# Optimization experiments

Hardware: AMD Instinct MI355X
Metric: run time of the kernel (lower is better)

Reference implementation:

```python
import jax, jax.numpy as jnp
import numpy as np


def setup_inputs() -> dict:
    key = jax.random.key(0)
    k1, k2 = jax.random.split(key)
    B, T, V = 256, 128, 512
    x = jax.random.normal(k1, (B, T, V), dtype=jnp.float32)
    targets = jax.random.randint(k2, (B, T), 0, V)
    return {"x": x, "targets": targets, "sup_batchsize": 256}


def reference(x, targets, sup_batchsize):
    # Faithful vectorization of InfoNCELoss.loss_fun (the per-i Python loop).
    x = jnp.clip(x, -30.0, 30.0)
    B, T, V = x.shape
    S = int(sup_batchsize)
    tgt = targets[:S]  # [S, T] target sequences used as positives/negatives

    # terms[i, b] = sum_t x[b, t, tgt[i, t]]  (gather each target sequence across the whole batch)
    gathered = jnp.take_along_axis(x[None], tgt[:, None, :, None], axis=3)  # [S, B, T, 1]
    terms = gathered[..., 0].sum(axis=-1)  # [S, B]

    denom = jax.nn.logsumexp(terms, axis=1)  # [S]
    numerators = terms[jnp.arange(S), jnp.arange(S)]  # terms[i, i] = own-sequence score
    losses = numerators - denom  # [S], per-row InfoNCE log-prob

    # coef[i, b] = 1{b == i} - softmax_b(terms[i, :])
    indicator = (jnp.arange(B)[None, :] == jnp.arange(S)[:, None]).astype(x.dtype)
    coef = indicator - jax.nn.softmax(terms, axis=1)  # [S, B]

    # grad[b, t, v] = sum_i 1{v == tgt[i, t]} * coef[i, b]  (scatter-add, no [S,T,V] one-hot)
    t_idx = jnp.arange(T)[None, :]  # broadcasts with tgt to [S, T]
    grad = jnp.zeros_like(x).at[:, t_idx, tgt].add(
        jnp.broadcast_to(coef.T[:, :, None], (B, S, T))
    )

    total_loss = losses.sum()  # InfoNCEFunction.forward returns sum(loss)
    return total_loss, grad
```

## Files before the change

kernel.cpp:

```cpp
#include <hip/hip_runtime.h>


#define TT 128
#define VV 512
#define QSPLIT 8
#define TQ (TT / QSPLIT)
#define TC 8

typedef float f4 __attribute__((ext_vector_type(4)));

__global__ __launch_bounds__(256) void terms_kernel(
    const float* __restrict__ x, const int* __restrict__ tgt,
    float* __restrict__ partial) {
  int bid = blockIdx.x;
  int b = bid & 255, q = bid >> 8, s = threadIdx.x;
  __shared__ __align__(16) float xch[TC * VV];
  const float* xb = x + ((size_t)b * TT + q * TQ) * VV;
  int4 tg[4];
#pragma unroll
  for (int k = 0; k < 4; ++k)
    tg[k] = ((const int4*)(tgt + (size_t)s * TT + q * TQ))[k];
  float acc = 0.f;
#pragma unroll
  for (int c = 0; c < 2; ++c) {
    const float4* src = (const float4*)(xb + c * TC * VV);
    float4* dst = (float4*)xch;
#pragma unroll
    for (int k = 0; k < 4; ++k) {
      float4 v = src[s + k * 256];
      v.x = fminf(fmaxf(v.x, -30.f), 30.f);
      v.y = fminf(fmaxf(v.y, -30.f), 30.f);
      v.z = fminf(fmaxf(v.z, -30.f), 30.f);
      v.w = fminf(fmaxf(v.w, -30.f), 30.f);
      dst[s + k * 256] = v;
    }
    __syncthreads();
    int4 a0 = tg[2 * c], a1 = tg[2 * c + 1];
    acc += xch[0 * VV + a0.x] + xch[1 * VV + a0.y] +
           xch[2 * VV + a0.z] + xch[3 * VV + a0.w] +
           xch[4 * VV + a1.x] + xch[5 * VV + a1.y] +
           xch[6 * VV + a1.z] + xch[7 * VV + a1.w];
    __syncthreads();
  }
  partial[(size_t)((q << 8) + b) * 256 + s] = acc;
}

__global__ __launch_bounds__(256) void softmax_kernel(
    const float* __restrict__ partial, float* __restrict__ coefT,
    float* __restrict__ losses) {
  int s = blockIdx.x, b = threadIdx.x;
  int w = b >> 6, lane = b & 63;
  float t = 0.f;
#pragma unroll
  for (int q = 0; q < QSPLIT; ++q)
    t += partial[(size_t)((q << 8) + b) * 256 + s];
  float m = t;
#pragma unroll
  for (int off = 32; off; off >>= 1) m = fmaxf(m, __shfl_xor(m, off));
  __shared__ float wm[4], ws[4];
  if (lane == 0) wm[w] = m;
  __syncthreads();
  m = fmaxf(fmaxf(wm[0], wm[1]), fmaxf(wm[2], wm[3]));
  float e = expf(t - m);
  float ss = e;
#pragma unroll
  for (int off = 32; off; off >>= 1) ss += __shfl_xor(ss, off);
  if (lane == 0) ws[w] = ss;
  __syncthreads();
  float sum = ws[0] + ws[1] + ws[2] + ws[3];
  coefT[(b << 8) + s] = (b == s ? 1.f : 0.f) - e / sum;
  if (b == s) losses[s] = (t - m) - logf(sum);
}

__global__ __launch_bounds__(256) void grad_kernel(
    const float* __restrict__ coefT, const int* __restrict__ tgt,
    const float* __restrict__ losses, float* __restrict__ out) {
  int j = blockIdx.x, s = threadIdx.x;
  int w = s >> 6, lane = s & 63;
  int b = j >> 4, t0 = (j & 15) << 3;
  __shared__ __align__(16) float rows[TC * VV + 1];
  __shared__ double dred[4];
  f4* rz = (f4*)rows;
  f4 zero = {0.f, 0.f, 0.f, 0.f};
#pragma unroll
  for (int k = 0; k < 4; ++k) rz[s + k * 256] = zero;
  if (s == 0) rows[TC * VV] = 0.f;

  float c = coefT[(b << 8) + s];
  int4 tg0 = *(const int4*)(tgt + (size_t)s * TT + t0);
  int4 tg1 = *(const int4*)(tgt + (size_t)s * TT + t0 + 4);

  float bc = 0.f;
  if (j > 0) {
    int R = j * 8 - 1;
    int bh = R >> 7, th = R & 127;
    if (tgt[(size_t)s * TT + th] == VV - 1) bc = coefT[(bh << 8) + s];
  }
  double ls = 0.0;
  if (j == 0) ls = (double)losses[s];

  __syncthreads();
  atomicAdd(&rows[1 + 0 * VV + tg0.x], c);
  atomicAdd(&rows[1 + 1 * VV + tg0.y], c);
  atomicAdd(&rows[1 + 2 * VV + tg0.z], c);
  atomicAdd(&rows[1 + 3 * VV + tg0.w], c);
  atomicAdd(&rows[1 + 4 * VV + tg1.x], c);
  atomicAdd(&rows[1 + 5 * VV + tg1.y], c);
  atomicAdd(&rows[1 + 6 * VV + tg1.z], c);
  atomicAdd(&rows[1 + 7 * VV + tg1.w], c);
#pragma unroll
  for (int off = 32; off; off >>= 1) bc += __shfl_xor(bc, off);
  if (j > 0 && lane == 0) atomicAdd(&rows[0], bc);
  if (j == 0) {
#pragma unroll
    for (int off = 32; off; off >>= 1) ls += __shfl_xor(ls, off);
    if (lane == 0) dred[w] = ls;
  }
  __syncthreads();
  if (j == 0 && s == 0) rows[0] = (float)(dred[0] + dred[1] + dred[2] + dred[3]);
  __syncthreads();

  f4* go = (f4*)(out + (size_t)j * 4096);
#pragma unroll
  for (int k = 0; k < 4; ++k)
    __builtin_nontemporal_store(rz[s + k * 256], &go[s + k * 256]);
  if (j == 4095 && s == 0) out[(size_t)4096 * 4096] = rows[TC * VV];
}

extern "C" void kernel_launch(void* const* d_in, const int* in_sizes, int n_in,
                              void* d_out, int out_size, void* d_ws, size_t ws_size,
                              hipStream_t stream) {
  const float* x = (const float*)d_in[0];
  const int* tgt = (const int*)d_in[1];
  float* out = (float*)d_out;

  float* partial = (float*)d_ws;
  float* coefT = partial + QSPLIT * 256 * 256;
  float* losses = coefT + 256 * 256;

  terms_kernel<<<dim3(2048), dim3(256), 0, stream>>>(x, tgt, partial);
  softmax_kernel<<<dim3(256), dim3(256), 0, stream>>>(partial, coefT, losses);
  grad_kernel<<<dim3(4096), dim3(256), 0, stream>>>(coefT, tgt, losses, out);
}
```

Baseline: 165.4 us.

## Fuse three kernels into one cooperative launch with grid syncs and LDS direct loads

```diff
diff --git a/kernel.cpp b/kernel.cpp
--- a/kernel.cpp
+++ b/kernel.cpp
@@ -1,4 +1,7 @@
 #include <hip/hip_runtime.h>
+#include <hip/hip_cooperative_groups.h>
+
+namespace cg = cooperative_groups;
 
 
 #define TT 128
@@ -8,6 +11,131 @@
 #define TC 8
 
 typedef float f4 __attribute__((ext_vector_type(4)));
+
+__device__ __forceinline__ float clip30(float v) {
+  return fminf(fmaxf(v, -30.f), 30.f);
+}
+
+__device__ __forceinline__ void gload16(const float* g, float* l) {
+  __builtin_amdgcn_global_load_lds(
+      (const __attribute__((address_space(1))) unsigned int*)g,
+      (__attribute__((address_space(3))) unsigned int*)l, 16, 0, 0);
+}
+
+__global__ __launch_bounds__(256) void fused_kernel(
+    const float* __restrict__ x, const int* __restrict__ tgt,
+    float* __restrict__ partial, float* __restrict__ coefT,
+    float* __restrict__ losses, float* __restrict__ out) {
+  cg::grid_group gg = cg::this_grid();
+  int bid = blockIdx.x, s = threadIdx.x;
+  int w = s >> 6, lane = s & 63;
+  __shared__ __align__(16) float smem[TC * VV + 1];
+  __shared__ double dred[4];
+  __shared__ float wred[8];
+
+  {
+    int b = bid & 255, q = bid >> 8;
+    const float* xb = x + ((size_t)b * TT + q * TQ) * VV;
+    int4 tg[4];
+#pragma unroll
+    for (int k = 0; k < 4; ++k)
+      tg[k] = ((const int4*)(tgt + (size_t)s * TT + q * TQ))[k];
+    float acc = 0.f;
+#pragma unroll
+    for (int c = 0; c < 2; ++c) {
+      const float* src = xb + c * TC * VV;
+#pragma unroll
+      for (int k = 0; k < 4; ++k)
+        gload16(src + 4 * (s + k * 256), &smem[4 * (s + k * 256)]);
+      __syncthreads();
+      int4 a0 = tg[2 * c], a1 = tg[2 * c + 1];
+      acc += clip30(smem[0 * VV + a0.x]) + clip30(smem[1 * VV + a0.y]) +
+             clip30(smem[2 * VV + a0.z]) + clip30(smem[3 * VV + a0.w]) +
+             clip30(smem[4 * VV + a1.x]) + clip30(smem[5 * VV + a1.y]) +
+             clip30(smem[6 * VV + a1.z]) + clip30(smem[7 * VV + a1.w]);
+      __syncthreads();
+    }
+    partial[(size_t)((q << 8) + b) * 256 + s] = acc;
+  }
+
+  gg.sync();
+
+  if (bid < 256) {
+    int row = bid, b = s;
+    float t = 0.f;
+#pragma unroll
+    for (int q = 0; q < QSPLIT; ++q)
+      t += partial[(size_t)((q << 8) + b) * 256 + row];
+    float m = t;
+#pragma unroll
+    for (int off = 32; off; off >>= 1) m = fmaxf(m, __shfl_xor(m, off));
+    if (lane == 0) wred[w] = m;
+    __syncthreads();
+    m = fmaxf(fmaxf(wred[0], wred[1]), fmaxf(wred[2], wred[3]));
+    float e = expf(t - m);
+    float ssum = e;
+#pragma unroll
+    for (int off = 32; off; off >>= 1) ssum += __shfl_xor(ssum, off);
+    if (lane == 0) wred[4 + w] = ssum;
+    __syncthreads();
+    float sum = wred[4] + wred[5] + wred[6] + wred[7];
+    coefT[(b << 8) + row] = (b == row ? 1.f : 0.f) - e / sum;
+    if (b == row) losses[row] = (t - m) - logf(sum);
+  }
+
+  gg.sync();
+
+#pragma unroll 1
+  for (int tt = 0; tt < 2; ++tt) {
+    int j = (bid << 1) | tt;
+    int b = j >> 4, t0 = (j & 15) << 3;
+    f4* rz = (f4*)smem;
+    f4 zero = {0.f, 0.f, 0.f, 0.f};
+#pragma unroll
+    for (int k = 0; k < 4; ++k) rz[s + k * 256] = zero;
+    if (s == 0) smem[TC * VV] = 0.f;
+
+    float c = coefT[(b << 8) + s];
+    int4 tg0 = *(const int4*)(tgt + (size_t)s * TT + t0);
+    int4 tg1 = *(const int4*)(tgt + (size_t)s * TT + t0 + 4);
+
+    float bc = 0.f;
+    if (j > 0) {
+      int R = j * 8 - 1;
+      int bh = R >> 7, th = R & 127;
+      if (tgt[(size_t)s * TT + th] == VV - 1) bc = coefT[(bh << 8) + s];
+    }
+    double ls = 0.0;
+    if (j == 0) ls = (double)losses[s];
+
+    __syncthreads();
+    atomicAdd(&smem[1 + 0 * VV + tg0.x], c);
+    atomicAdd(&smem[1 + 1 * VV + tg0.y], c);
+    atomicAdd(&smem[1 + 2 * VV + tg0.z], c);
+    atomicAdd(&smem[1 + 3 * VV + tg0.w], c);
+    atomicAdd(&smem[1 + 4 * VV + tg1.x], c);
+    atomicAdd(&smem[1 + 5 * VV + tg1.y], c);
+    atomicAdd(&smem[1 + 6 * VV + tg1.z], c);
+    atomicAdd(&smem[1 + 7 * VV + tg1.w], c);
+#pragma unroll
+    for (int off = 32; off; off >>= 1) bc += __shfl_xor(bc, off);
+    if (j > 0 && lane == 0) atomicAdd(&smem[0], bc);
+    if (j == 0) {
+#pragma unroll
+      for (int off = 32; off; off >>= 1) ls += __shfl_xor(ls, off);
+      if (lane == 0) dred[w] = ls;
+    }
+    __syncthreads();
+    if (j == 0 && s == 0) smem[0] = (float)(dred[0] + dred[1] + dred[2] + dred[3]);
+    __syncthreads();
+
+    f4* go = (f4*)(out + (size_t)j * 4096);
+#pragma unroll
+    for (int k = 0; k < 4; ++k)
+      __builtin_nontemporal_store(rz[s + k * 256], &go[s + k * 256]);
+    if (j == 4095 && s == 0) out[(size_t)4096 * 4096] = smem[TC * VV];
+  }
+}
 
 __global__ __launch_bounds__(256) void terms_kernel(
     const float* __restrict__ x, const int* __restrict__ tgt,
@@ -23,23 +151,16 @@
   float acc = 0.f;
 #pragma unroll
   for (int c = 0; c < 2; ++c) {
-    const float4* src = (const float4*)(xb + c * TC * VV);
-    float4* dst = (float4*)xch;
-#pragma unroll
-    for (int k = 0; k < 4; ++k) {
-      float4 v = src[s + k * 256];
-      v.x = fminf(fmaxf(v.x, -30.f), 30.f);
-      v.y = fminf(fmaxf(v.y, -30.f), 30.f);
-      v.z = fminf(fmaxf(v.z, -30.f), 30.f);
-      v.w = fminf(fmaxf(v.w, -30.f), 30.f);
-      dst[s + k * 256] = v;
-    }
+    const float* src = xb + c * TC * VV;
+#pragma unroll
+    for (int k = 0; k < 4; ++k)
+      gload16(src + 4 * (s + k * 256), &xch[4 * (s + k * 256)]);
     __syncthreads();
     int4 a0 = tg[2 * c], a1 = tg[2 * c + 1];
-    acc += xch[0 * VV + a0.x] + xch[1 * VV + a0.y] +
-           xch[2 * VV + a0.z] + xch[3 * VV + a0.w] +
-           xch[4 * VV + a1.x] + xch[5 * VV + a1.y] +
-           xch[6 * VV + a1.z] + xch[7 * VV + a1.w];
+    acc += clip30(xch[0 * VV + a0.x]) + clip30(xch[1 * VV + a0.y]) +
+           clip30(xch[2 * VV + a0.z]) + clip30(xch[3 * VV + a0.w]) +
+           clip30(xch[4 * VV + a1.x]) + clip30(xch[5 * VV + a1.y]) +
+           clip30(xch[6 * VV + a1.z]) + clip30(xch[7 * VV + a1.w]);
     __syncthreads();
   }
   partial[(size_t)((q << 8) + b) * 256 + s] = acc;
@@ -48,12 +169,12 @@
 __global__ __launch_bounds__(256) void softmax_kernel(
     const float* __restrict__ partial, float* __restrict__ coefT,
     float* __restrict__ losses) {
-  int s = blockIdx.x, b = threadIdx.x;
+  int row = blockIdx.x, b = threadIdx.x;
   int w = b >> 6, lane = b & 63;
   float t = 0.f;
 #pragma unroll
   for (int q = 0; q < QSPLIT; ++q)
-    t += partial[(size_t)((q << 8) + b) * 256 + s];
+    t += partial[(size_t)((q << 8) + b) * 256 + row];
   float m = t;
 #pragma unroll
   for (int off = 32; off; off >>= 1) m = fmaxf(m, __shfl_xor(m, off));
@@ -62,14 +183,14 @@
   __syncthreads();
   m = fmaxf(fmaxf(wm[0], wm[1]), fmaxf(wm[2], wm[3]));
   float e = expf(t - m);
-  float ss = e;
-#pragma unroll
-  for (int off = 32; off; off >>= 1) ss += __shfl_xor(ss, off);
-  if (lane == 0) ws[w] = ss;
+  float ssum = e;
+#pragma unroll
+  for (int off = 32; off; off >>= 1) ssum += __shfl_xor(ssum, off);
+  if (lane == 0) ws[w] = ssum;
   __syncthreads();
   float sum = ws[0] + ws[1] + ws[2] + ws[3];
-  coefT[(b << 8) + s] = (b == s ? 1.f : 0.f) - e / sum;
-  if (b == s) losses[s] = (t - m) - logf(sum);
+  coefT[(b << 8) + row] = (b == row ? 1.f : 0.f) - e / sum;
+  if (b == row) losses[row] = (t - m) - logf(sum);
 }
 
 __global__ __launch_bounds__(256) void grad_kernel(
@@ -138,7 +259,13 @@
   float* coefT = partial + QSPLIT * 256 * 256;
   float* losses = coefT + 256 * 256;
 
-  terms_kernel<<<dim3(2048), dim3(256), 0, stream>>>(x, tgt, partial);
-  softmax_kernel<<<dim3(256), dim3(256), 0, stream>>>(partial, coefT, losses);
-  grad_kernel<<<dim3(4096), dim3(256), 0, stream>>>(coefT, tgt, losses, out);
-}
+  void* args[] = {(void*)&x, (void*)&tgt, (void*)&partial,
+                  (void*)&coefT, (void*)&losses, (void*)&out};
+  hipError_t err = hipLaunchCooperativeKernel(
+      (const void*)fused_kernel, dim3(2048), dim3(256), args, 0, stream);
+  if (err != hipSuccess) {
+    terms_kernel<<<dim3(2048), dim3(256), 0, stream>>>(x, tgt, partial);
+    softmax_kernel<<<dim3(256), dim3(256), 0, stream>>>(partial, coefT, losses);
+    grad_kernel<<<dim3(4096), dim3(256), 0, stream>>>(coefT, tgt, losses, out);
+  }
+}
```

Measured after the change: 640.3 us. 3.87x slower.

## Gather terms directly from global memory and enlarge grad tiles to 16 rows

Applied to the files above, without the earlier changes.

```diff
diff --git a/kernel.cpp b/kernel.cpp
--- a/kernel.cpp
+++ b/kernel.cpp
@@ -5,55 +5,43 @@
 #define VV 512
 #define QSPLIT 8
 #define TQ (TT / QSPLIT)
-#define TC 8
 
 typedef float f4 __attribute__((ext_vector_type(4)));
+
+__device__ __forceinline__ float clip30(float v) {
+  return fminf(fmaxf(v, -30.f), 30.f);
+}
 
 __global__ __launch_bounds__(256) void terms_kernel(
     const float* __restrict__ x, const int* __restrict__ tgt,
     float* __restrict__ partial) {
   int bid = blockIdx.x;
   int b = bid & 255, q = bid >> 8, s = threadIdx.x;
-  __shared__ __align__(16) float xch[TC * VV];
-  const float* xb = x + ((size_t)b * TT + q * TQ) * VV;
   int4 tg[4];
 #pragma unroll
   for (int k = 0; k < 4; ++k)
     tg[k] = ((const int4*)(tgt + (size_t)s * TT + q * TQ))[k];
-  float acc = 0.f;
+  const float* xb = x + ((size_t)b * TT + q * TQ) * VV;
+  float a0 = 0.f, a1 = 0.f, a2 = 0.f, a3 = 0.f;
 #pragma unroll
-  for (int c = 0; c < 2; ++c) {
-    const float4* src = (const float4*)(xb + c * TC * VV);
-    float4* dst = (float4*)xch;
-#pragma unroll
-    for (int k = 0; k < 4; ++k) {
-      float4 v = src[s + k * 256];
-      v.x = fminf(fmaxf(v.x, -30.f), 30.f);
-      v.y = fminf(fmaxf(v.y, -30.f), 30.f);
-      v.z = fminf(fmaxf(v.z, -30.f), 30.f);
-      v.w = fminf(fmaxf(v.w, -30.f), 30.f);
-      dst[s + k * 256] = v;
-    }
-    __syncthreads();
-    int4 a0 = tg[2 * c], a1 = tg[2 * c + 1];
-    acc += xch[0 * VV + a0.x] + xch[1 * VV + a0.y] +
-           xch[2 * VV + a0.z] + xch[3 * VV + a0.w] +
-           xch[4 * VV + a1.x] + xch[5 * VV + a1.y] +
-           xch[6 * VV + a1.z] + xch[7 * VV + a1.w];
-    __syncthreads();
+  for (int k = 0; k < 4; ++k) {
+    a0 += clip30(xb[(4 * k + 0) * VV + tg[k].x]);
+    a1 += clip30(xb[(4 * k + 1) * VV + tg[k].y]);
+    a2 += clip30(xb[(4 * k + 2) * VV + tg[k].z]);
+    a3 += clip30(xb[(4 * k + 3) * VV + tg[k].w]);
   }
-  partial[(size_t)((q << 8) + b) * 256 + s] = acc;
+  partial[(size_t)((q << 8) + b) * 256 + s] = (a0 + a1) + (a2 + a3);
 }
 
 __global__ __launch_bounds__(256) void softmax_kernel(
     const float* __restrict__ partial, float* __restrict__ coefT,
     float* __restrict__ losses) {
-  int s = blockIdx.x, b = threadIdx.x;
+  int row = blockIdx.x, b = threadIdx.x;
   int w = b >> 6, lane = b & 63;
   float t = 0.f;
 #pragma unroll
   for (int q = 0; q < QSPLIT; ++q)
-    t += partial[(size_t)((q << 8) + b) * 256 + s];
+    t += partial[(size_t)((q << 8) + b) * 256 + row];
   float m = t;
 #pragma unroll
   for (int off = 32; off; off >>= 1) m = fmaxf(m, __shfl_xor(m, off));
@@ -62,69 +50,72 @@
   __syncthreads();
   m = fmaxf(fmaxf(wm[0], wm[1]), fmaxf(wm[2], wm[3]));
   float e = expf(t - m);
-  float ss = e;
+  float ssum = e;
 #pragma unroll
-  for (int off = 32; off; off >>= 1) ss += __shfl_xor(ss, off);
-  if (lane == 0) ws[w] = ss;
+  for (int off = 32; off; off >>= 1) ssum += __shfl_xor(ssum, off);
+  if (lane == 0) ws[w] = ssum;
   __syncthreads();
   float sum = ws[0] + ws[1] + ws[2] + ws[3];
-  coefT[(b << 8) + s] = (b == s ? 1.f : 0.f) - e / sum;
-  if (b == s) losses[s] = (t - m) - logf(sum);
+  coefT[(b << 8) + row] = (b == row ? 1.f : 0.f) - e / sum;
+  if (b == row) losses[row] = (t - m) - logf(sum);
 }
 
 __global__ __launch_bounds__(256) void grad_kernel(
     const float* __restrict__ coefT, const int* __restrict__ tgt,
     const float* __restrict__ losses, float* __restrict__ out) {
-  int j = blockIdx.x, s = threadIdx.x;
+  int k = blockIdx.x, s = threadIdx.x;
   int w = s >> 6, lane = s & 63;
-  int b = j >> 4, t0 = (j & 15) << 3;
-  __shared__ __align__(16) float rows[TC * VV + 1];
+  int b = k >> 3, t0 = (k & 7) << 4;
+  __shared__ __align__(16) float smem[16 * VV + 1];
   __shared__ double dred[4];
-  f4* rz = (f4*)rows;
+
+  float c = coefT[(b << 8) + s];
+  int4 tg[4];
+#pragma unroll
+  for (int m = 0; m < 4; ++m)
+    tg[m] = ((const int4*)(tgt + (size_t)s * TT + t0))[m];
+  float bc = 0.f;
+  double ls = 0.0;
+  if (k > 0) {
+    int R = (k << 4) - 1;
+    int bh = R >> 7, th = R & 127;
+    if (tgt[(size_t)s * TT + th] == VV - 1) bc = coefT[(bh << 8) + s];
+  } else {
+    ls = (double)losses[s];
+  }
+
+  f4* rz = (f4*)smem;
   f4 zero = {0.f, 0.f, 0.f, 0.f};
 #pragma unroll
-  for (int k = 0; k < 4; ++k) rz[s + k * 256] = zero;
-  if (s == 0) rows[TC * VV] = 0.f;
+  for (int m = 0; m < 8; ++m) rz[s + m * 256] = zero;
+  if (s == 0) smem[16 * VV] = 0.f;
+  __syncthreads();
 
-  float c = coefT[(b << 8) + s];
-  int4 tg0 = *(const int4*)(tgt + (size_t)s * TT + t0);
-  int4 tg1 = *(const int4*)(tgt + (size_t)s * TT + t0 + 4);
-
-  float bc = 0.f;
-  if (j > 0) {
-    int R = j * 8 - 1;
-    int bh = R >> 7, th = R & 127;
-    if (tgt[(size_t)s * TT + th] == VV - 1) bc = coefT[(bh << 8) + s];
+#pragma unroll
+  for (int m = 0; m < 4; ++m) {
+    atomicAdd(&smem[1 + (4 * m + 0) * VV + tg[m].x], c);
+    atomicAdd(&smem[1 + (4 * m + 1) * VV + tg[m].y], c);
+    atomicAdd(&smem[1 + (4 * m + 2) * VV + tg[m].z], c);
+    atomicAdd(&smem[1 + (4 * m + 3) * VV + tg[m].w], c);
   }
-  double ls = 0.0;
-  if (j == 0) ls = (double)losses[s];
-
-  __syncthreads();
-  atomicAdd(&rows[1 + 0 * VV + tg0.x], c);
-  atomicAdd(&rows[1 + 1 * VV + tg0.y], c);
-  atomicAdd(&rows[1 + 2 * VV + tg0.z], c);
-  atomicAdd(&rows[1 + 3 * VV + tg0.w], c);
-  atomicAdd(&rows[1 + 4 * VV + tg1.x], c);
-  atomicAdd(&rows[1 + 5 * VV + tg1.y], c);
-  atomicAdd(&rows[1 + 6 * VV + tg1.z], c);
-  atomicAdd(&rows[1 + 7 * VV + tg1.w], c);
 #pragma unroll
   for (int off = 32; off; off >>= 1) bc += __shfl_xor(bc, off);
-  if (j > 0 && lane == 0) atomicAdd(&rows[0], bc);
-  if (j == 0) {
+  if (k > 0 && lane == 0) atomicAdd(&smem[0], bc);
+  if (k == 0) {
 #pragma unroll
     for (int off = 32; off; off >>= 1) ls += __shfl_xor(ls, off);
     if (lane == 0) dred[w] = ls;
   }
   __syncthreads();
-  if (j == 0 && s == 0) rows[0] = (float)(dred[0] + dred[1] + dred[2] + dred[3]);
-  __syncthreads();
 
-  f4* go = (f4*)(out + (size_t)j * 4096);
+  if (k == 0 && s == 0)
+    smem[0] = (float)(dred[0] + dred[1] + dred[2] + dred[3]);
+
+  f4* go = (f4*)(out + (size_t)k * 8192);
 #pragma unroll
-  for (int k = 0; k < 4; ++k)
-    __builtin_nontemporal_store(rz[s + k * 256], &go[s + k * 256]);
-  if (j == 4095 && s == 0) out[(size_t)4096 * 4096] = rows[TC * VV];
+  for (int m = 0; m < 8; ++m)
+    __builtin_nontemporal_store(rz[s + m * 256], &go[s + m * 256]);
+  if (k == 2047 && s == 0) out[(size_t)4096 * 4096] = smem[16 * VV];
 }
 
 extern "C" void kernel_launch(void* const* d_in, const int* in_sizes, int n_in,
@@ -140,5 +131,5 @@
 
   terms_kernel<<<dim3(2048), dim3(256), 0, stream>>>(x, tgt, partial);
   softmax_kernel<<<dim3(256), dim3(256), 0, stream>>>(partial, coefT, losses);
-  grad_kernel<<<dim3(4096), dim3(256), 0, stream>>>(coefT, tgt, losses, out);
+  grad_kernel<<<dim3(2048), dim3(256), 0, stream>>>(coefT, tgt, losses, out);
 }
```

Measured after the change: 166.6 us. No clear change (+0.7%).
